# Kernel optimization log

Hardware: AMD Instinct MI355X
Metric: run time of the kernel (lower is better)

## Reference

```python
import jax, jax.numpy as jnp
import numpy as np

NUM_NODES = 10000
NUM_FEAT = 32
HIDDEN = 64
OUT_FEAT = 16
NUM_EDGES = 160000
SEQ_LEN = 12
BATCH = 1


def _gcn_conv(x, W, b, row, col, n):
    # PyG GCNConv: h = D^-1/2 (A+I) D^-1/2 (x @ W) + b
    # x: (n, T, F_in), row/col: (E+n,) with self-loops already appended
    h = x @ W                                              # (n, T, H)
    deg = jax.ops.segment_sum(jnp.ones_like(col, dtype=h.dtype), col, num_segments=n)
    dis = 1.0 / jnp.sqrt(jnp.maximum(deg, 1.0))            # deg >= 1 due to self-loops
    norm = dis[row] * dis[col]                             # (E+n,)
    msg = h[row] * norm[:, None, None]                     # gather + scale
    return jax.ops.segment_sum(msg, col, num_segments=n) + b


def _lstm_layer(x, wih, whh, bih, bhh):
    # x: (N, T, F); PyTorch gate order i, f, g, o
    H = whh.shape[1]
    Nn = x.shape[0]
    bias = bih + bhh

    def step(carry, xt):
        h, c = carry
        g = xt @ wih.T + h @ whh.T + bias
        i, f, gg, o = jnp.split(g, 4, axis=-1)
        c = jax.nn.sigmoid(f) * c + jax.nn.sigmoid(i) * jnp.tanh(gg)
        h = jax.nn.sigmoid(o) * jnp.tanh(c)
        return (h, c), h

    h0 = jnp.zeros((Nn, H), x.dtype)
    c0 = jnp.zeros((Nn, H), x.dtype)
    _, ys = jax.lax.scan(step, (h0, c0), jnp.transpose(x, (1, 0, 2)))
    return jnp.transpose(ys, (1, 0, 2))                    # (N, T, H)


def setup_inputs() -> dict:
    key = jax.random.key(0)
    ks = jax.random.split(key, 16)
    s_in = 1.0 / np.sqrt(NUM_FEAT)
    s_h = 1.0 / np.sqrt(HIDDEN)
    inp = {
        "x": jax.random.normal(ks[0], (BATCH, SEQ_LEN, NUM_NODES, NUM_FEAT), jnp.float32),
        "edge_index": jax.random.randint(ks[1], (2, NUM_EDGES), 0, NUM_NODES, dtype=jnp.int64),
        "gw0": jax.random.normal(ks[2], (NUM_FEAT, HIDDEN), jnp.float32) * s_in,
        "gb0": jnp.zeros((HIDDEN,), jnp.float32),
        "gw1": jax.random.normal(ks[3], (HIDDEN, HIDDEN), jnp.float32) * s_h,
        "gb1": jnp.zeros((HIDDEN,), jnp.float32),
        "wih0": jax.random.normal(ks[4], (4 * HIDDEN, HIDDEN), jnp.float32) * s_h,
        "whh0": jax.random.normal(ks[5], (4 * HIDDEN, HIDDEN), jnp.float32) * s_h,
        "bih0": jax.random.normal(ks[6], (4 * HIDDEN,), jnp.float32) * s_h,
        "bhh0": jax.random.normal(ks[7], (4 * HIDDEN,), jnp.float32) * s_h,
        "wih1": jax.random.normal(ks[8], (4 * HIDDEN, HIDDEN), jnp.float32) * s_h,
        "whh1": jax.random.normal(ks[9], (4 * HIDDEN, HIDDEN), jnp.float32) * s_h,
        "bih1": jax.random.normal(ks[10], (4 * HIDDEN,), jnp.float32) * s_h,
        "bhh1": jax.random.normal(ks[11], (4 * HIDDEN,), jnp.float32) * s_h,
        "fc_w": jax.random.normal(ks[12], (OUT_FEAT, HIDDEN), jnp.float32) * s_h,
        "fc_b": jnp.zeros((OUT_FEAT,), jnp.float32),
    }
    return inp


def reference(x, edge_index, gw0, gb0, gw1, gb1, wih0, whh0, bih0, bhh0,
              wih1, whh1, bih1, bhh1, fc_w, fc_b):
    B, T, n, F = x.shape
    BN = B * n
    # (B, T, N, F) -> (B, N, T, F) -> (B*N, T, F); the per-timestep GCN loop in
    # the original is batched over T here (same math, edge_index is time-invariant).
    xs = jnp.transpose(x, (0, 2, 1, 3)).reshape(BN, T, F)
    loops = jnp.arange(BN, dtype=edge_index.dtype)
    row = jnp.concatenate([edge_index[0], loops])
    col = jnp.concatenate([edge_index[1], loops])
    h = jax.nn.relu(_gcn_conv(xs, gw0, gb0, row, col, BN))
    h = jax.nn.relu(_gcn_conv(h, gw1, gb1, row, col, BN))
    h = _lstm_layer(h, wih0, whh0, bih0, bhh0)
    h = _lstm_layer(h, wih1, whh1, bih1, bhh1)
    out = h[:, -1, :] @ fc_w.T + fc_b                      # last timestep only
    return out.reshape(B, n, OUT_FEAT)
```

## Files before the change

### kernel.cpp

```cpp
#include <hip/hip_runtime.h>
#include <hip/hip_bf16.h>

constexpr int kNN  = 10000;
constexpr int kTT  = 12;
constexpr int kFIN = 32;
constexpr int kHH  = 64;
constexpr int kH4  = 256;
constexpr int kOUT = 16;
constexpr int kNE  = 160000;

typedef _Float16 half8 __attribute__((ext_vector_type(8)));
typedef _Float16 half4 __attribute__((ext_vector_type(4)));
typedef _Float16 half2t __attribute__((ext_vector_type(2)));
typedef float floatx4 __attribute__((ext_vector_type(4)));

__device__ __forceinline__ float sigf(float x){ return 1.f/(1.f+__expf(-x)); }
__device__ __forceinline__ float tanh_fast(float x){
  float xc = fminf(fmaxf(x,-30.f),30.f);
  float e = __expf(-2.f*xc);
  return (1.f-e)/(1.f+e);
}

__global__ void k_detect_cast(const int* __restrict__ ei, int* __restrict__ anyf,
                              const float* __restrict__ x, _Float16* __restrict__ xh){
  int a = 0;
  for (int i = blockIdx.x*256 + threadIdx.x; i < kNE; i += gridDim.x*256)
    a |= ei[2*i+1];
  unsigned long long m = __ballot(a != 0);
  if ((threadIdx.x & 63) == 0 && m) atomicOr(anyf, 1);
  const int NV = kNN*kTT*kFIN/4;
  for (int i = blockIdx.x*256 + threadIdx.x; i < NV; i += gridDim.x*256){
    float4 v = *(const float4*)&x[4*i];
    half4 h;
    h[0]=(_Float16)v.x; h[1]=(_Float16)v.y; h[2]=(_Float16)v.z; h[3]=(_Float16)v.w;
    *(half4*)&xh[4*i] = h;
  }
}

__global__ void k_deg(const int* __restrict__ ei, const int* __restrict__ anyf,
                      int* __restrict__ cnt){
  int e = blockIdx.x*256 + threadIdx.x;
  if (e >= kNE) return;
  int c = (anyf[0]==0) ? ei[2*(kNE+e)] : ei[kNE+e];
  atomicAdd(&cnt[c], 1);
}

__global__ void k_scan(const int* __restrict__ cnt, int* __restrict__ offs,
                       float* __restrict__ dis){
  __shared__ int wsum[4];
  int tid = threadIdx.x;
  const int CH = (kNN + 255)/256;
  int lo = tid*CH, hi = min(lo+CH, kNN);
  int s = 0;
  for (int i = lo; i < hi; ++i) s += cnt[i];
  int orig = s;
  int lane = tid & 63, wv = tid >> 6;
  #pragma unroll
  for (int d = 1; d < 64; d <<= 1){
    int v = __shfl_up(s, d, 64);
    if (lane >= d) s += v;
  }
  if (lane == 63) wsum[wv] = s;
  __syncthreads();
  int add = 0;
  for (int k2 = 0; k2 < wv; ++k2) add += wsum[k2];
  int run = s - orig + add;
  for (int i = lo; i < hi; ++i){ offs[i] = run; run += cnt[i]; }
  if (hi == kNN) offs[kNN] = run;
  for (int i = tid; i < kNN; i += 256) dis[i] = rsqrtf((float)(cnt[i]+1));
}

__global__ void k_scatter(const int* __restrict__ ei, const int* __restrict__ anyf,
                          const int* __restrict__ offs, int* __restrict__ cur,
                          const float* __restrict__ dis,
                          int2* __restrict__ edat){
  int e = blockIdx.x*256 + threadIdx.x;
  if (e >= kNE) return;
  int f = (anyf[0]==0);
  int r = f ? ei[2*e]         : ei[e];
  int c = f ? ei[2*(kNE+e)]   : ei[kNE+e];
  int p = offs[c] + atomicAdd(&cur[c], 1);
  edat[p] = make_int2(r, __float_as_int(dis[r]*dis[c]));
}

template<int F>
__global__ __launch_bounds__(256) void k_agg(const _Float16* __restrict__ hin,
                     _Float16* __restrict__ hout,
                     const float* __restrict__ dis,
                     const int* __restrict__ offs, const int2* __restrict__ edat){
  constexpr int LPF = F/2;
  constexpr int TPW = 64/LPF;
  int wid = threadIdx.x >> 6, lane = threadIdx.x & 63;
  int gw = blockIdx.x*4 + wid;
  int tq = gw / kNN, n = gw - tq*kNN;
  int fp = lane & (LPF-1), tsub = lane / LPF;
  int t = TPW*tq + tsub;
  const _Float16* hb = hin + (size_t)t*kNN*F;
  float d = dis[n], ws = d*d;
  half2t sv = *(const half2t*)&hb[(size_t)n*F + 2*fp];
  float a0 = ws*(float)sv[0], a1 = ws*(float)sv[1];
  int e0 = __builtin_amdgcn_readfirstlane(offs[n]);
  int e1 = __builtin_amdgcn_readfirstlane(offs[n+1]);
  int e = e0;
  for (; e + 8 <= e1; e += 8){
    int2 d8[8];
    #pragma unroll
    for (int u = 0; u < 8; ++u) d8[u] = edat[e+u];
    half2t v[8];
    #pragma unroll
    for (int u = 0; u < 8; ++u) v[u] = *(const half2t*)&hb[(size_t)d8[u].x*F + 2*fp];
    #pragma unroll
    for (int u = 0; u < 8; ++u){
      float wu = __int_as_float(d8[u].y);
      a0 = fmaf(wu, (float)v[u][0], a0);
      a1 = fmaf(wu, (float)v[u][1], a1);
    }
  }
  for (; e < e1; ++e){
    int2 du = edat[e];
    float wu = __int_as_float(du.y);
    half2t vu = *(const half2t*)&hb[(size_t)du.x*F + 2*fp];
    a0 = fmaf(wu, (float)vu[0], a0);
    a1 = fmaf(wu, (float)vu[1], a1);
  }
  half2t o; o[0] = (_Float16)a0; o[1] = (_Float16)a1;
  *(half2t*)&hout[((size_t)t*kNN + n)*F + 2*fp] = o;
}

template<int K, int N, bool NM>
__global__ __launch_bounds__(256) void k_gemm(const _Float16* __restrict__ in,
                      const float* __restrict__ Wg, const float* __restrict__ bias,
                      _Float16* __restrict__ out){
  constexpr int COLG = N/4;
  constexpr int ROWG = 256/COLG;
  constexpr int MR   = 4;
  constexpr int MTILE= ROWG*MR;
  constexpr int AP   = K + 4;
  __shared__ float Wl[K*N];
  __shared__ float Al[MTILE*AP];
  int tid = threadIdx.x;
  int m0 = blockIdx.x*MTILE;
  for (int idx = tid; idx < MTILE*K/8; idx += 256){
    int r = idx/(K/8), k8 = idx - r*(K/8);
    half8 v = *(const half8*)&in[(size_t)(m0 + r)*K + k8*8];
    float* dst = &Al[r*AP + k8*8];
    #pragma unroll
    for (int j = 0; j < 8; ++j) dst[j] = (float)v[j];
  }
  for (int idx = tid; idx < K*N; idx += 256) Wl[idx] = Wg[idx];
  __syncthreads();
  int cg = tid % COLG, rg = tid / COLG;
  int c0 = cg*4, r0 = rg*MR;
  float acc[MR][4];
  #pragma unroll
  for (int r=0;r<MR;++r){acc[r][0]=0.f;acc[r][1]=0.f;acc[r][2]=0.f;acc[r][3]=0.f;}
  #pragma unroll 2
  for (int k = 0; k < K; k += 4){
    float4 wv[4];
    #pragma unroll
    for (int kk = 0; kk < 4; ++kk) wv[kk] = *(const float4*)&Wl[(k+kk)*N + c0];
    #pragma unroll
    for (int r = 0; r < MR; ++r){
      float4 a4 = *(const float4*)&Al[(r0+r)*AP + k];
      acc[r][0] = fmaf(a4.x, wv[0].x, acc[r][0]);
      acc[r][1] = fmaf(a4.x, wv[0].y, acc[r][1]);
      acc[r][2] = fmaf(a4.x, wv[0].z, acc[r][2]);
      acc[r][3] = fmaf(a4.x, wv[0].w, acc[r][3]);
      acc[r][0] = fmaf(a4.y, wv[1].x, acc[r][0]);
      acc[r][1] = fmaf(a4.y, wv[1].y, acc[r][1]);
      acc[r][2] = fmaf(a4.y, wv[1].z, acc[r][2]);
      acc[r][3] = fmaf(a4.y, wv[1].w, acc[r][3]);
      acc[r][0] = fmaf(a4.z, wv[2].x, acc[r][0]);
      acc[r][1] = fmaf(a4.z, wv[2].y, acc[r][1]);
      acc[r][2] = fmaf(a4.z, wv[2].z, acc[r][2]);
      acc[r][3] = fmaf(a4.z, wv[2].w, acc[r][3]);
      acc[r][0] = fmaf(a4.w, wv[3].x, acc[r][0]);
      acc[r][1] = fmaf(a4.w, wv[3].y, acc[r][1]);
      acc[r][2] = fmaf(a4.w, wv[3].z, acc[r][2]);
      acc[r][3] = fmaf(a4.w, wv[3].w, acc[r][3]);
    }
  }
  float4 bb = *(const float4*)&bias[c0];
  #pragma unroll
  for (int r = 0; r < MR; ++r){
    half4 hv;
    hv[0]=(_Float16)fmaxf(acc[r][0]+bb.x, 0.f);
    hv[1]=(_Float16)fmaxf(acc[r][1]+bb.y, 0.f);
    hv[2]=(_Float16)fmaxf(acc[r][2]+bb.z, 0.f);
    hv[3]=(_Float16)fmaxf(acc[r][3]+bb.w, 0.f);
    int m = m0 + r0 + r;
    size_t oi;
    if (NM){ int t = m/kNN, n = m - t*kNN; oi = ((size_t)n*kTT + t)*N + c0; }
    else    oi = (size_t)m*N + c0;
    *(half4*)&out[oi] = hv;
  }
}

__global__ __launch_bounds__(256) void k_rec3(const _Float16* __restrict__ xin,
                     const float* __restrict__ wih0, const float* __restrict__ whh0,
                     const float* __restrict__ bih0, const float* __restrict__ bhh0,
                     const float* __restrict__ wih1, const float* __restrict__ whh1,
                     const float* __restrict__ bih1, const float* __restrict__ bhh1,
                     const float* __restrict__ fcw, const float* __restrict__ fcb,
                     float* __restrict__ out){
  constexpr int XP  = kTT*kHH + 8;
  constexpr int LPH = 72;
  __shared__ _Float16 xl[16*XP];
  __shared__ _Float16 h0l[16*LPH];
  __shared__ _Float16 h1l[16*LPH];
  int tid = threadIdx.x, w = tid >> 6, lane = tid & 63;
  int lo = lane & 15, hi4 = lane >> 4;
  int nb = blockIdx.x*16;

  for (int idx = tid; idx < 16*(kTT*kHH/8); idx += 256){
    int r = idx/(kTT*kHH/8), c8 = idx - r*(kTT*kHH/8);
    *(half8*)&xl[r*XP + c8*8] = *(const half8*)&xin[((size_t)(nb+r)*kTT*kHH) + c8*8];
  }

  half8 BI0[4][2], BH0[4][2], BI1[4][2], BH1[4][2];
  float bias0[4], bias1[4];
  #pragma unroll
  for (int g4 = 0; g4 < 4; ++g4){
    int row = g4*kHH + w*16 + lo;
    bias0[g4] = bih0[row] + bhh0[row];
    bias1[g4] = bih1[row] + bhh1[row];
    #pragma unroll
    for (int kt = 0; kt < 2; ++kt){
      const float* p0 = wih0 + (size_t)row*kHH + kt*32 + hi4*8;
      const float* q0 = whh0 + (size_t)row*kHH + kt*32 + hi4*8;
      const float* p1 = wih1 + (size_t)row*kHH + kt*32 + hi4*8;
      const float* q1 = whh1 + (size_t)row*kHH + kt*32 + hi4*8;
      half8 a, b, c2, d2;
      #pragma unroll
      for (int j = 0; j < 8; ++j){
        a[j]=(_Float16)p0[j]; b[j]=(_Float16)q0[j];
        c2[j]=(_Float16)p1[j]; d2[j]=(_Float16)q1[j];
      }
      BI0[g4][kt]=a; BH0[g4][kt]=b; BI1[g4][kt]=c2; BH1[g4][kt]=d2;
    }
  }
  half8 FW[2];
  if (w == 0){
    #pragma unroll
    for (int kt = 0; kt < 2; ++kt){
      const float* pf = fcw + (size_t)lo*kHH + kt*32 + hi4*8;
      half8 f;
      #pragma unroll
      for (int j = 0; j < 8; ++j) f[j] = (_Float16)pf[j];
      FW[kt] = f;
    }
  }

  float c0s[4] = {0.f,0.f,0.f,0.f}, c1s[4] = {0.f,0.f,0.f,0.f};
  half8 ah0[2], ah1[2];
  __syncthreads();

  for (int t = 0; t < kTT; ++t){
    half8 ax0 = *(const half8*)&xl[lo*XP + t*kHH + hi4*8];
    half8 ax1 = *(const half8*)&xl[lo*XP + t*kHH + 32 + hi4*8];
    floatx4 acc[4];
    #pragma unroll
    for (int g4 = 0; g4 < 4; ++g4){
      floatx4 a = {0.f,0.f,0.f,0.f};
      a = __builtin_amdgcn_mfma_f32_16x16x32_f16(ax0, BI0[g4][0], a, 0,0,0);
      a = __builtin_amdgcn_mfma_f32_16x16x32_f16(ax1, BI0[g4][1], a, 0,0,0);
      acc[g4] = a;
    }
    if (t > 0){
      #pragma unroll
      for (int g4 = 0; g4 < 4; ++g4){
        floatx4 a = acc[g4];
        a = __builtin_amdgcn_mfma_f32_16x16x32_f16(ah0[0], BH0[g4][0], a, 0,0,0);
        a = __builtin_amdgcn_mfma_f32_16x16x32_f16(ah0[1], BH0[g4][1], a, 0,0,0);
        acc[g4] = a;
      }
    }
    #pragma unroll
    for (int r = 0; r < 4; ++r){
      float gi = acc[0][r] + bias0[0];
      float gf = acc[1][r] + bias0[1];
      float gg = acc[2][r] + bias0[2];
      float go = acc[3][r] + bias0[3];
      float ii = sigf(gi), ff = sigf(gf), gt = tanh_fast(gg), oo = sigf(go);
      c0s[r] = ff*c0s[r] + ii*gt;
      float hn = oo * tanh_fast(c0s[r]);
      h0l[(hi4*4 + r)*LPH + w*16 + lo] = (_Float16)hn;
    }
    __syncthreads();
    #pragma unroll
    for (int kt = 0; kt < 2; ++kt)
      ah0[kt] = *(const half8*)&h0l[lo*LPH + kt*32 + hi4*8];

    #pragma unroll
    for (int g4 = 0; g4 < 4; ++g4){
      floatx4 a = {0.f,0.f,0.f,0.f};
      a = __builtin_amdgcn_mfma_f32_16x16x32_f16(ah0[0], BI1[g4][0], a, 0,0,0);
      a = __builtin_amdgcn_mfma_f32_16x16x32_f16(ah0[1], BI1[g4][1], a, 0,0,0);
      acc[g4] = a;
    }
    if (t > 0){
      #pragma unroll
      for (int g4 = 0; g4 < 4; ++g4){
        floatx4 a = acc[g4];
        a = __builtin_amdgcn_mfma_f32_16x16x32_f16(ah1[0], BH1[g4][0], a, 0,0,0);
        a = __builtin_amdgcn_mfma_f32_16x16x32_f16(ah1[1], BH1[g4][1], a, 0,0,0);
        acc[g4] = a;
      }
    }
    #pragma unroll
    for (int r = 0; r < 4; ++r){
      float gi = acc[0][r] + bias1[0];
      float gf = acc[1][r] + bias1[1];
      float gg = acc[2][r] + bias1[2];
      float go = acc[3][r] + bias1[3];
      float ii = sigf(gi), ff = sigf(gf), gt = tanh_fast(gg), oo = sigf(go);
      c1s[r] = ff*c1s[r] + ii*gt;
      float hn = oo * tanh_fast(c1s[r]);
      h1l[(hi4*4 + r)*LPH + w*16 + lo] = (_Float16)hn;
    }
    __syncthreads();
    #pragma unroll
    for (int kt = 0; kt < 2; ++kt)
      ah1[kt] = *(const half8*)&h1l[lo*LPH + kt*32 + hi4*8];
  }

  if (w == 0){
    floatx4 a = {0.f,0.f,0.f,0.f};
    a = __builtin_amdgcn_mfma_f32_16x16x32_f16(ah1[0], FW[0], a, 0,0,0);
    a = __builtin_amdgcn_mfma_f32_16x16x32_f16(ah1[1], FW[1], a, 0,0,0);
    float bo = fcb[lo];
    #pragma unroll
    for (int r = 0; r < 4; ++r)
      out[(size_t)(nb + hi4*4 + r)*kOUT + lo] = a[r] + bo;
  }
}

extern "C" void kernel_launch(void* const* d_in, const int* in_sizes, int n_in,
                              void* d_out, int out_size, void* d_ws, size_t ws_size,
                              hipStream_t stream){
  const float* x    = (const float*)d_in[0];
  const int*   ei   = (const int*)  d_in[1];
  const float* gw0  = (const float*)d_in[2];
  const float* gb0  = (const float*)d_in[3];
  const float* gw1  = (const float*)d_in[4];
  const float* gb1  = (const float*)d_in[5];
  const float* wih0 = (const float*)d_in[6];
  const float* whh0 = (const float*)d_in[7];
  const float* bih0 = (const float*)d_in[8];
  const float* bhh0 = (const float*)d_in[9];
  const float* wih1 = (const float*)d_in[10];
  const float* whh1 = (const float*)d_in[11];
  const float* bih1 = (const float*)d_in[12];
  const float* bhh1 = (const float*)d_in[13];
  const float* fcw  = (const float*)d_in[14];
  const float* fcb  = (const float*)d_in[15];
  float* out = (float*)d_out;

  char* ws = (char*)d_ws;
  size_t p = 0;
  auto carve = [&](size_t bytes)->char*{
    char* r = ws + p;
    p += (bytes + 255) & ~(size_t)255;
    return r;
  };
  int*   anyf = (int*)  carve(256);
  int*   cnt  = (int*)  carve(sizeof(int)*kNN);
  int*   cur  = (int*)  carve(sizeof(int)*kNN);
  size_t zbytes = p;
  int*   offs = (int*)  carve(sizeof(int)*(kNN+1));
  float* dis  = (float*)carve(sizeof(float)*kNN);
  int2*  edat = (int2*) carve(sizeof(int2)*kNE);
  _Float16* xh   = (_Float16*)carve(sizeof(_Float16)*(size_t)kNN*kTT*kFIN);
  _Float16* aggX = (_Float16*)carve(sizeof(_Float16)*(size_t)kNN*kTT*kFIN);
  _Float16* bufA = (_Float16*)carve(sizeof(_Float16)*(size_t)kNN*kTT*kHH);
  _Float16* bufB = (_Float16*)carve(sizeof(_Float16)*(size_t)kNN*kTT*kHH);
  (void)ws_size; (void)in_sizes; (void)n_in; (void)out_size;

  hipMemsetAsync(ws, 0, zbytes, stream);
  k_detect_cast<<<120, 256, 0, stream>>>(ei, anyf, x, xh);
  k_deg    <<<(kNE+255)/256, 256, 0, stream>>>(ei, anyf, cnt);
  k_scan   <<<1, 256, 0, stream>>>(cnt, offs, dis);
  k_scatter<<<(kNE+255)/256, 256, 0, stream>>>(ei, anyf, offs, cur, dis, edat);

  k_agg<kFIN><<<(kNN*(kTT/4))/4, 256, 0, stream>>>(xh, aggX, dis, offs, edat);
  k_gemm<kFIN, kHH, false><<<(kNN*kTT)/64, 256, 0, stream>>>(aggX, gw0, gb0, bufB);
  k_agg<kHH><<<(kNN*(kTT/2))/4, 256, 0, stream>>>(bufB, bufA, dis, offs, edat);
  k_gemm<kHH, kHH, true><<<(kNN*kTT)/64, 256, 0, stream>>>(bufA, gw1, gb1, bufB);

  k_rec3<<<kNN/16, 256, 0, stream>>>(bufB, wih0, whh0, bih0, bhh0,
                                     wih1, whh1, bih1, bhh1, fcw, fcb, out);
}
```

Measured before the change: 330.6 us.

## Split fused two-layer LSTM into per-layer kernels with one wave per node tile

Replaces the fused two-layer recurrent kernel, where four waves split the gate columns of a 16-node tile and sync through shared memory every step, with a per-layer kernel. In the new kernel each wave owns a whole 16-node tile and computes all 256 gate columns, so the per-step block barriers disappear. Input weights are held in registers, recurrent weights are read from LDS as pre-laid-out fragments, and the next timestep's input is prefetched from global memory. The cost is an extra launch and a round trip of the layer-0 hidden sequence through global memory, plus heavy register pressure from 32 half8 weight fragments per lane.

```diff
diff --git a/kernel.cpp b/kernel.cpp
--- a/kernel.cpp
+++ b/kernel.cpp
@@ -196,54 +196,61 @@
   }
 }
 
-__global__ __launch_bounds__(256) void k_rec3(const _Float16* __restrict__ xin,
-                     const float* __restrict__ wih0, const float* __restrict__ whh0,
-                     const float* __restrict__ bih0, const float* __restrict__ bhh0,
-                     const float* __restrict__ wih1, const float* __restrict__ whh1,
-                     const float* __restrict__ bih1, const float* __restrict__ bhh1,
+__device__ __forceinline__ void stage_frags(const float* __restrict__ W,
+                                            _Float16* __restrict__ dst,
+                                            int tid, int nthr){
+  for (int idx = tid; idx < 2048; idx += nthr){
+    int fi = idx >> 6, ln = idx & 63;
+    int g = fi >> 1, kt = fi & 1;
+    const float* s = W + (size_t)(g*16 + (ln & 15))*kHH + kt*32 + ((ln >> 4) << 3);
+    half8 v;
+    #pragma unroll
+    for (int j = 0; j < 8; ++j) v[j] = (_Float16)s[j];
+    *(half8*)&dst[(size_t)idx*8] = v;
+  }
+}
+
+template<bool LAST>
+__global__ __launch_bounds__(128) void k_lstm(const _Float16* __restrict__ xin,
+                     const float* __restrict__ wih, const float* __restrict__ whh,
+                     const float* __restrict__ bih, const float* __restrict__ bhh,
                      const float* __restrict__ fcw, const float* __restrict__ fcb,
-                     float* __restrict__ out){
-  constexpr int XP  = kTT*kHH + 8;
-  constexpr int LPH = 72;
-  __shared__ _Float16 xl[16*XP];
-  __shared__ _Float16 h0l[16*LPH];
-  __shared__ _Float16 h1l[16*LPH];
+                     void* __restrict__ outp){
+  __shared__ _Float16 WL[16384];
+  __shared__ float    biasL[kH4];
+  __shared__ _Float16 hs[2][1152];
   int tid = threadIdx.x, w = tid >> 6, lane = tid & 63;
-  int lo = lane & 15, hi4 = lane >> 4;
-  int nb = blockIdx.x*16;
-
-  for (int idx = tid; idx < 16*(kTT*kHH/8); idx += 256){
-    int r = idx/(kTT*kHH/8), c8 = idx - r*(kTT*kHH/8);
-    *(half8*)&xl[r*XP + c8*8] = *(const half8*)&xin[((size_t)(nb+r)*kTT*kHH) + c8*8];
-  }
-
-  half8 BI0[4][2], BH0[4][2], BI1[4][2], BH1[4][2];
-  float bias0[4], bias1[4];
-  #pragma unroll
-  for (int g4 = 0; g4 < 4; ++g4){
-    int row = g4*kHH + w*16 + lo;
-    bias0[g4] = bih0[row] + bhh0[row];
-    bias1[g4] = bih1[row] + bhh1[row];
+  int lo = lane & 15, quad = lane >> 4;
+  int tile = blockIdx.x*2 + w;
+  int nb = tile*16;
+
+  stage_frags(wih, WL, tid, 128);
+  __syncthreads();
+  half8 WihF[16][2];
+  #pragma unroll
+  for (int g = 0; g < 16; ++g){
+    #pragma unroll
+    for (int kt = 0; kt < 2; ++kt)
+      WihF[g][kt] = *(const half8*)&WL[(size_t)((g*2+kt)*64 + lane)*8];
+  }
+  __syncthreads();
+  stage_frags(whh, WL, tid, 128);
+  for (int i = tid; i < kH4; i += 128) biasL[i] = bih[i] + bhh[i];
+  __syncthreads();
+  if (tile >= kNN/16) return;
+
+  float bias_v[4][4];
+  #pragma unroll
+  for (int gg = 0; gg < 4; ++gg)
+    #pragma unroll
+    for (int q = 0; q < 4; ++q)
+      bias_v[gg][q] = biasL[q*64 + gg*16 + lo];
+
+  half8 FW[2];
+  if (LAST){
     #pragma unroll
     for (int kt = 0; kt < 2; ++kt){
-      const float* p0 = wih0 + (size_t)row*kHH + kt*32 + hi4*8;
-      const float* q0 = whh0 + (size_t)row*kHH + kt*32 + hi4*8;
-      const float* p1 = wih1 + (size_t)row*kHH + kt*32 + hi4*8;
-      const float* q1 = whh1 + (size_t)row*kHH + kt*32 + hi4*8;
-      half8 a, b, c2, d2;
-      #pragma unroll
-      for (int j = 0; j < 8; ++j){
-        a[j]=(_Float16)p0[j]; b[j]=(_Float16)q0[j];
-        c2[j]=(_Float16)p1[j]; d2[j]=(_Float16)q1[j];
-      }
-      BI0[g4][kt]=a; BH0[g4][kt]=b; BI1[g4][kt]=c2; BH1[g4][kt]=d2;
-    }
-  }
-  half8 FW[2];
-  if (w == 0){
-    #pragma unroll
-    for (int kt = 0; kt < 2; ++kt){
-      const float* pf = fcw + (size_t)lo*kHH + kt*32 + hi4*8;
+      const float* pf = fcw + (size_t)lo*kHH + kt*32 + quad*8;
       half8 f;
       #pragma unroll
       for (int j = 0; j < 8; ++j) f[j] = (_Float16)pf[j];
@@ -251,87 +258,79 @@
     }
   }
 
-  float c0s[4] = {0.f,0.f,0.f,0.f}, c1s[4] = {0.f,0.f,0.f,0.f};
-  half8 ah0[2], ah1[2];
-  __syncthreads();
+  const _Float16* xr = xin + (size_t)(nb + lo)*kTT*kHH;
+  _Float16* sc = &hs[w][0];
+  floatx4 cst[4];
+  #pragma unroll
+  for (int gg = 0; gg < 4; ++gg) cst[gg] = (floatx4){0.f,0.f,0.f,0.f};
+  half8 ah0, ah1;
+  half8 axn0 = *(const half8*)&xr[quad*8];
+  half8 axn1 = *(const half8*)&xr[32 + quad*8];
 
   for (int t = 0; t < kTT; ++t){
-    half8 ax0 = *(const half8*)&xl[lo*XP + t*kHH + hi4*8];
-    half8 ax1 = *(const half8*)&xl[lo*XP + t*kHH + 32 + hi4*8];
-    floatx4 acc[4];
-    #pragma unroll
-    for (int g4 = 0; g4 < 4; ++g4){
-      floatx4 a = {0.f,0.f,0.f,0.f};
-      a = __builtin_amdgcn_mfma_f32_16x16x32_f16(ax0, BI0[g4][0], a, 0,0,0);
-      a = __builtin_amdgcn_mfma_f32_16x16x32_f16(ax1, BI0[g4][1], a, 0,0,0);
-      acc[g4] = a;
-    }
-    if (t > 0){
-      #pragma unroll
-      for (int g4 = 0; g4 < 4; ++g4){
-        floatx4 a = acc[g4];
-        a = __builtin_amdgcn_mfma_f32_16x16x32_f16(ah0[0], BH0[g4][0], a, 0,0,0);
-        a = __builtin_amdgcn_mfma_f32_16x16x32_f16(ah0[1], BH0[g4][1], a, 0,0,0);
-        acc[g4] = a;
-      }
-    }
-    #pragma unroll
-    for (int r = 0; r < 4; ++r){
-      float gi = acc[0][r] + bias0[0];
-      float gf = acc[1][r] + bias0[1];
-      float gg = acc[2][r] + bias0[2];
-      float go = acc[3][r] + bias0[3];
-      float ii = sigf(gi), ff = sigf(gf), gt = tanh_fast(gg), oo = sigf(go);
-      c0s[r] = ff*c0s[r] + ii*gt;
-      float hn = oo * tanh_fast(c0s[r]);
-      h0l[(hi4*4 + r)*LPH + w*16 + lo] = (_Float16)hn;
-    }
-    __syncthreads();
-    #pragma unroll
-    for (int kt = 0; kt < 2; ++kt)
-      ah0[kt] = *(const half8*)&h0l[lo*LPH + kt*32 + hi4*8];
-
-    #pragma unroll
-    for (int g4 = 0; g4 < 4; ++g4){
-      floatx4 a = {0.f,0.f,0.f,0.f};
-      a = __builtin_amdgcn_mfma_f32_16x16x32_f16(ah0[0], BI1[g4][0], a, 0,0,0);
-      a = __builtin_amdgcn_mfma_f32_16x16x32_f16(ah0[1], BI1[g4][1], a, 0,0,0);
-      acc[g4] = a;
-    }
-    if (t > 0){
-      #pragma unroll
-      for (int g4 = 0; g4 < 4; ++g4){
-        floatx4 a = acc[g4];
-        a = __builtin_amdgcn_mfma_f32_16x16x32_f16(ah1[0], BH1[g4][0], a, 0,0,0);
-        a = __builtin_amdgcn_mfma_f32_16x16x32_f16(ah1[1], BH1[g4][1], a, 0,0,0);
-        acc[g4] = a;
-      }
-    }
-    #pragma unroll
-    for (int r = 0; r < 4; ++r){
-      float gi = acc[0][r] + bias1[0];
-      float gf = acc[1][r] + bias1[1];
-      float gg = acc[2][r] + bias1[2];
-      float go = acc[3][r] + bias1[3];
-      float ii = sigf(gi), ff = sigf(gf), gt = tanh_fast(gg), oo = sigf(go);
-      c1s[r] = ff*c1s[r] + ii*gt;
-      float hn = oo * tanh_fast(c1s[r]);
-      h1l[(hi4*4 + r)*LPH + w*16 + lo] = (_Float16)hn;
-    }
-    __syncthreads();
-    #pragma unroll
-    for (int kt = 0; kt < 2; ++kt)
-      ah1[kt] = *(const half8*)&h1l[lo*LPH + kt*32 + hi4*8];
-  }
-
-  if (w == 0){
+    half8 ax0 = axn0, ax1 = axn1;
+    if (t < kTT-1){
+      axn0 = *(const half8*)&xr[(size_t)(t+1)*kHH + quad*8];
+      axn1 = *(const half8*)&xr[(size_t)(t+1)*kHH + 32 + quad*8];
+    }
+    #pragma unroll
+    for (int gg = 0; gg < 4; ++gg){
+      floatx4 acc[4];
+      #pragma unroll
+      for (int q = 0; q < 4; ++q){
+        float b = bias_v[gg][q];
+        acc[q] = (floatx4){b, b, b, b};
+      }
+      #pragma unroll
+      for (int q = 0; q < 4; ++q){
+        int ga = q*4 + gg;
+        acc[q] = __builtin_amdgcn_mfma_f32_16x16x32_f16(ax0, WihF[ga][0], acc[q], 0,0,0);
+        acc[q] = __builtin_amdgcn_mfma_f32_16x16x32_f16(ax1, WihF[ga][1], acc[q], 0,0,0);
+      }
+      if (t > 0){
+        #pragma unroll
+        for (int q = 0; q < 4; ++q){
+          int ga = q*4 + gg;
+          half8 w0 = *(const half8*)&WL[(size_t)((ga*2+0)*64 + lane)*8];
+          half8 w1 = *(const half8*)&WL[(size_t)((ga*2+1)*64 + lane)*8];
+          acc[q] = __builtin_amdgcn_mfma_f32_16x16x32_f16(ah0, w0, acc[q], 0,0,0);
+          acc[q] = __builtin_amdgcn_mfma_f32_16x16x32_f16(ah1, w1, acc[q], 0,0,0);
+        }
+      }
+      #pragma unroll
+      for (int r = 0; r < 4; ++r){
+        float ii = sigf(acc[0][r]);
+        float ff = sigf(acc[1][r]);
+        float gt = tanh_fast(acc[2][r]);
+        float oo = sigf(acc[3][r]);
+        float cc = ff*cst[gg][r] + ii*gt;
+        cst[gg][r] = cc;
+        float hv = oo * tanh_fast(cc);
+        sc[(quad*4 + r)*72 + gg*16 + lo] = (_Float16)hv;
+      }
+    }
+    ah0 = *(const half8*)&sc[lo*72 + quad*8];
+    ah1 = *(const half8*)&sc[lo*72 + 32 + quad*8];
+    if (!LAST){
+      _Float16* hout = (_Float16*)outp;
+      #pragma unroll
+      for (int k2 = 0; k2 < 2; ++k2){
+        int node = (lane >> 3) + 8*k2;
+        int cell = (lane & 7)*8;
+        half8 hvv = *(const half8*)&sc[node*72 + cell];
+        *(half8*)&hout[(size_t)(nb+node)*kTT*kHH + (size_t)t*kHH + cell] = hvv;
+      }
+    }
+  }
+  if (LAST){
+    float* out = (float*)outp;
     floatx4 a = {0.f,0.f,0.f,0.f};
-    a = __builtin_amdgcn_mfma_f32_16x16x32_f16(ah1[0], FW[0], a, 0,0,0);
-    a = __builtin_amdgcn_mfma_f32_16x16x32_f16(ah1[1], FW[1], a, 0,0,0);
+    a = __builtin_amdgcn_mfma_f32_16x16x32_f16(ah0, FW[0], a, 0,0,0);
+    a = __builtin_amdgcn_mfma_f32_16x16x32_f16(ah1, FW[1], a, 0,0,0);
     float bo = fcb[lo];
     #pragma unroll
     for (int r = 0; r < 4; ++r)
-      out[(size_t)(nb + hi4*4 + r)*kOUT + lo] = a[r] + bo;
+      out[(size_t)(nb + quad*4 + r)*kOUT + lo] = a[r] + bo;
   }
 }
 
@@ -387,6 +386,8 @@
   k_agg<kHH><<<(kNN*(kTT/2))/4, 256, 0, stream>>>(bufB, bufA, dis, offs, edat);
   k_gemm<kHH, kHH, true><<<(kNN*kTT)/64, 256, 0, stream>>>(bufA, gw1, gb1, bufB);
 
-  k_rec3<<<kNN/16, 256, 0, stream>>>(bufB, wih0, whh0, bih0, bhh0,
-                                     wih1, whh1, bih1, bhh1, fcw, fcb, out);
-}
+  k_lstm<false><<<(kNN/16 + 1)/2, 128, 0, stream>>>(bufB, wih0, whh0, bih0, bhh0,
+                                                    nullptr, nullptr, bufA);
+  k_lstm<true ><<<(kNN/16 + 1)/2, 128, 0, stream>>>(bufA, wih1, whh1, bih1, bhh1,
+                                                    fcw, fcb, out);
+}
```

Result: slower. 346.1 us (+4.7%).
